# Kernel optimization log

Measured on AMD Instinct MI355X. Metric: run time of the kernel, lower is better.

Reference implementation:

```python
import jax, jax.numpy as jnp
import numpy as np

D_MODEL = 2048
N_HEADS = 16
D_K = D_MODEL // N_HEADS
MAX_SEQ = 2048
THETA = 10000.0


def _rope(x, token_positions):
    # x: [B, H, S, d_k], token_positions: [S] int
    freqs = 1.0 / THETA ** (jnp.arange(0, D_K, 2, dtype=jnp.float32) / D_K)  # [d_k/2]
    angles = token_positions.astype(jnp.float32)[:, None] * freqs[None, :]   # [S, d_k/2]
    cos, sin = jnp.cos(angles), jnp.sin(angles)
    x_even, x_odd = x[..., 0::2], x[..., 1::2]
    out_even = x_even * cos - x_odd * sin
    out_odd = x_even * sin + x_odd * cos
    return jnp.stack([out_even, out_odd], axis=-1).reshape(x.shape)


def setup_inputs() -> dict:
    key = jax.random.key(0)
    ks = jax.random.split(key, 5)
    B, S = 2, 2048
    std = np.sqrt(2.0 / (D_MODEL + D_MODEL))
    def w(k):
        return (jax.random.truncated_normal(k, -3.0, 3.0, (D_MODEL, D_MODEL), jnp.float32) * std)
    return {
        "x": jax.random.normal(ks[0], (B, S, D_MODEL), jnp.float32),
        "wq": w(ks[1]), "wk": w(ks[2]), "wv": w(ks[3]), "wo": w(ks[4]),
        "token_positions": jnp.arange(S, dtype=jnp.int32),
    }


def reference(x, wq, wk, wv, wo, token_positions):
    B, S, _ = x.shape
    # Linear: einsum('... i, o i -> ... o')
    def proj(w):
        h = jnp.einsum('bsi,oi->bso', x, w)
        return h.reshape(B, S, N_HEADS, D_K).transpose(0, 2, 1, 3)  # [B,H,S,d_k]
    Q, K, V = proj(wq), proj(wk), proj(wv)
    Q = _rope(Q, token_positions)
    K = _rope(K, token_positions)
    scores = jnp.einsum('bhqd,bhkd->bhqk', Q, K) / jnp.sqrt(jnp.float32(D_K))
    causal = jnp.tril(jnp.ones((S, S), dtype=bool))
    scores = jnp.where(causal, scores, -jnp.inf)
    attn = jax.nn.softmax(scores, axis=-1)
    out = jnp.einsum('bhqk,bhkd->bhqd', attn, V)
    out = out.transpose(0, 2, 1, 3).reshape(B, S, D_MODEL)
    return jnp.einsum('bsi,oi->bso', out, wo)
```

## Files before the change

### kernel.cpp

```cpp
#include <hip/hip_runtime.h>
#include <stdint.h>
#include <stddef.h>

typedef unsigned short u16;
typedef unsigned int u32;
typedef __attribute__((ext_vector_type(8))) short s8v;
typedef __attribute__((ext_vector_type(4))) short s4v;
typedef __attribute__((ext_vector_type(4))) float f4v;

#define D_MODEL 2048
#define NH 16
#define DK 128

__device__ __forceinline__ float b2f(u16 u) {
    union { u32 i; float f; } v; v.i = ((u32)u) << 16; return v.f;
}
__device__ __forceinline__ u16 f2b(float f) {
    u32 u = __builtin_bit_cast(u32, f);
    u32 r = (u + 0x7fffu + ((u >> 16) & 1u)) >> 16;
    return (u16)r;
}
__device__ __forceinline__ float fexp2(float x) {
    return __builtin_amdgcn_exp2f(x);
}
__device__ __forceinline__ f4v mfma16(s8v a, s8v b, f4v c) {
    return __builtin_amdgcn_mfma_f32_16x16x32_bf16(a, b, c, 0, 0, 0);
}
__device__ __forceinline__ void gload_lds16(const void* g, void* l) {
    __builtin_amdgcn_global_load_lds(
        (const __attribute__((address_space(1))) u32*)(uintptr_t)g,
        (__attribute__((address_space(3))) u32*)(uintptr_t)l, 16, 0, 0);
}

__device__ __forceinline__ void store_out(u16* p, float v)   { *p = f2b(v); }
__device__ __forceinline__ void store_out(float* p, float v) { *p = v; }

#define SBAR()   asm volatile("s_barrier" ::: "memory")
#define VMCNT(n) asm volatile("s_waitcnt vmcnt(" #n ")" ::: "memory")

__global__ __launch_bounds__(256) void cvt_bf16(
    const float* __restrict__ s0, const float* __restrict__ s1,
    const float* __restrict__ s2, const float* __restrict__ s3,
    const float* __restrict__ s4,
    u16* __restrict__ d0, u16* __restrict__ d1, u16* __restrict__ d2,
    u16* __restrict__ d3, u16* __restrict__ d4,
    int n0, int nw)
{
    const int seg = blockIdx.y;
    const float* s = (seg == 0) ? s0 : (seg == 1) ? s1 : (seg == 2) ? s2 : (seg == 3) ? s3 : s4;
    u16*         d = (seg == 0) ? d0 : (seg == 1) ? d1 : (seg == 2) ? d2 : (seg == 3) ? d3 : d4;
    const int    n = (seg == 0) ? n0 : nw;
    int i = (blockIdx.x * 256 + threadIdx.x) * 8;
    if (i >= n) return;
    f4v a = *(const f4v*)(s + i);
    f4v b = *(const f4v*)(s + i + 4);
    s8v o;
    o[0] = (short)f2b(a[0]); o[1] = (short)f2b(a[1]);
    o[2] = (short)f2b(a[2]); o[3] = (short)f2b(a[3]);
    o[4] = (short)f2b(b[0]); o[5] = (short)f2b(b[1]);
    o[6] = (short)f2b(b[2]); o[7] = (short)f2b(b[3]);
    *(s8v*)(d + i) = o;
}

__global__ __launch_bounds__(512) void gemm256(
    const u16* __restrict__ A,
    const u16* __restrict__ B0, const u16* __restrict__ B1,
    u16* __restrict__ C0, u16* __restrict__ C1,
    int M, int N, int K)
{
    const int z = blockIdx.z;
    const u16* Bp = (z == 0) ? B0 : B1;
    u16*       Cp = (z == 0) ? C0 : C1;

    __shared__ short As[2 * 256 * 64];
    __shared__ short Bs[2 * 256 * 64];

    const int t    = threadIdx.x;
    const int lane = t & 63;
    const int w    = t >> 6;
    const int wr   = w >> 2;
    const int wc   = w & 3;
    const int m0   = blockIdx.x * 256;
    const int n0   = blockIdx.y * 256;

    const int srow = t >> 3;
    const int scol = (((t & 7) ^ ((t >> 3) & 7)) * 8);

    const u16* gA = A  + (size_t)(m0 + srow) * K + scol;
    const u16* gB = Bp + (size_t)(n0 + srow) * K + scol;
    char* lA = (char*)As + (size_t)w * 1024;
    char* lB = (char*)Bs + (size_t)w * 1024;
    const size_t rstep = (size_t)64 * K;

    const int fr = lane & 15;
    const int g4 = lane >> 4;
    const int xa = fr & 7;

    f4v acc[8][4];
#pragma unroll
    for (int i = 0; i < 8; i++)
#pragma unroll
        for (int j = 0; j < 4; j++) acc[i][j] = (f4v){0.f, 0.f, 0.f, 0.f};

    auto stageA = [&](int p, int kt, int h) {
        const u16* g = gA + (size_t)kt * 64;
#pragma unroll
        for (int j = 0; j < 2; j++)
            gload_lds16(g + (size_t)(2 * h + j) * rstep,
                        lA + p * 32768 + (2 * h + j) * 8192);
    };
    auto stageB = [&](int p, int kt, int h) {
        const u16* g = gB + (size_t)kt * 64;
#pragma unroll
        for (int j = 0; j < 2; j++)
            gload_lds16(g + (size_t)(2 * h + j) * rstep,
                        lB + p * 32768 + (2 * h + j) * 8192);
    };
    auto loadA = [&](int p, int mh, int ks, s8v* aF) {
        const short* base = As + p * 16384;
        const int sl = ((ks * 4 + g4) ^ xa) * 8;
#pragma unroll
        for (int mi = 0; mi < 4; mi++)
            aF[mi] = *(const s8v*)&base[(wr * 128 + mh * 64 + mi * 16 + fr) * 64 + sl];
    };
    auto loadB = [&](int p, int ks, s8v* bF) {
        const short* base = Bs + p * 16384;
        const int sl = ((ks * 4 + g4) ^ xa) * 8;
#pragma unroll
        for (int ni = 0; ni < 4; ni++)
            bF[ni] = *(const s8v*)&base[(wc * 64 + ni * 16 + fr) * 64 + sl];
    };
    auto mfc = [&](int mh, s8v* aF, s8v* bF) {
        __builtin_amdgcn_s_setprio(1);
#pragma unroll
        for (int mi = 0; mi < 4; mi++)
#pragma unroll
            for (int ni = 0; ni < 4; ni++)
                acc[mh * 4 + mi][ni] = mfma16(aF[mi], bF[ni], acc[mh * 4 + mi][ni]);
        __builtin_amdgcn_s_setprio(0);
    };

    const int NT = K / 64;
    const int NI = NT / 2;

    stageB(0, 0, 0); stageB(0, 0, 1); stageA(0, 0, 0); stageA(0, 0, 1);
    stageB(1, 1, 0);
    VMCNT(2);
    SBAR();

    for (int i = 0; i < NI; i++) {
        const int k1 = 2 * i + 1;
        const int k2 = (2 * i + 2 < NT) ? 2 * i + 2 : 0;
        const int k3 = (2 * i + 3 < NT) ? 2 * i + 3 : 1;
        s8v aF[4], bF[4];

        loadA(0, 0, 0, aF); loadB(0, 0, bF);
        stageB(1, k1, 1);
        VMCNT(4); SBAR();
        mfc(0, aF, bF);
        SBAR();
        loadA(0, 1, 0, aF);
        stageA(1, k1, 0);
        SBAR();
        mfc(1, aF, bF);
        SBAR();
        loadA(0, 0, 1, aF); loadB(0, 1, bF);
        stageA(1, k1, 1);
        SBAR();
        mfc(0, aF, bF);
        SBAR();
        loadA(0, 1, 1, aF);
        stageB(0, k2, 0);
        VMCNT(2); SBAR();
        mfc(1, aF, bF);
        SBAR();
        loadA(1, 0, 0, aF); loadB(1, 0, bF);
        stageB(0, k2, 1);
        VMCNT(4); SBAR();
        mfc(0, aF, bF);
        SBAR();
        loadA(1, 1, 0, aF);
        stageA(0, k2, 0);
        SBAR();
        mfc(1, aF, bF);
        SBAR();
        loadA(1, 0, 1, aF); loadB(1, 1, bF);
        stageA(0, k2, 1);
        SBAR();
        mfc(0, aF, bF);
        SBAR();
        loadA(1, 1, 1, aF);
        stageB(1, k3, 0);
        VMCNT(2); SBAR();
        mfc(1, aF, bF);
        SBAR();
    }
    VMCNT(0);

    const int rg = g4 * 4;
#pragma unroll
    for (int mit = 0; mit < 8; mit++)
#pragma unroll
        for (int ni = 0; ni < 4; ni++) {
            size_t base = (size_t)(m0 + wr * 128 + mit * 16 + rg) * N
                        + (n0 + wc * 64 + ni * 16 + fr);
#pragma unroll
            for (int r = 0; r < 4; r++)
                Cp[base + (size_t)r * N] = f2b(acc[mit][ni][r]);
        }
}

template<typename OutT, int MODE>
__global__ __launch_bounds__(512) void gemm128(
    const u16* __restrict__ A, const u16* __restrict__ Bp,
    OutT* __restrict__ Cp, int M, int N, int K, int Sdim)
{
    __shared__ short As[3 * 256 * 64];
    __shared__ short Bs[3 * 128 * 64];

    const int t    = threadIdx.x;
    const int lane = t & 63;
    const int w    = t >> 6;
    const int wr   = w >> 1;
    const int wc   = w & 1;
    const int m0   = blockIdx.x * 256;
    const int n0   = blockIdx.y * 128;

    const int srow = t >> 3;
    const int scol = (((t & 7) ^ ((t >> 3) & 7)) * 8);

    const u16* gA = A  + (size_t)(m0 + srow) * K + scol;
    const u16* gB = Bp + (size_t)(n0 + srow) * K + scol;
    char* lA = (char*)As + (size_t)w * 1024;
    char* lB = (char*)Bs + (size_t)w * 1024;
    const size_t rstep = (size_t)64 * K;

    const int fr = lane & 15;
    const int g4 = lane >> 4;
    const int xa = fr & 7;

    f4v acc[4][4];
#pragma unroll
    for (int i = 0; i < 4; i++)
#pragma unroll
        for (int j = 0; j < 4; j++) acc[i][j] = (f4v){0.f, 0.f, 0.f, 0.f};

    auto stageA = [&](int p, int kt, int h) {
        const u16* g = gA + (size_t)kt * 64;
#pragma unroll
        for (int j = 0; j < 2; j++)
            gload_lds16(g + (size_t)(2 * h + j) * rstep,
                        lA + p * 32768 + (2 * h + j) * 8192);
    };
    auto stageB = [&](int p, int kt) {
        const u16* g = gB + (size_t)kt * 64;
#pragma unroll
        for (int j = 0; j < 2; j++)
            gload_lds16(g + (size_t)j * rstep,
                        lB + p * 16384 + j * 8192);
    };
    auto loadA = [&](int p, int mh, int ks, s8v* aF) {
        const short* base = As + p * 16384;
        const int sl = ((ks * 4 + g4) ^ xa) * 8;
#pragma unroll
        for (int j = 0; j < 2; j++)
            aF[j] = *(const s8v*)&base[(wr * 64 + (mh * 2 + j) * 16 + fr) * 64 + sl];
    };
    auto loadB = [&](int p, int ks, s8v* bF) {
        const short* base = Bs + p * 8192;
        const int sl = ((ks * 4 + g4) ^ xa) * 8;
#pragma unroll
        for (int ni = 0; ni < 4; ni++)
            bF[ni] = *(const s8v*)&base[(wc * 64 + ni * 16 + fr) * 64 + sl];
    };
    auto mfc = [&](int mh, s8v* aF, s8v* bF) {
        __builtin_amdgcn_s_setprio(1);
#pragma unroll
        for (int j = 0; j < 2; j++)
#pragma unroll
            for (int ni = 0; ni < 4; ni++)
                acc[mh * 2 + j][ni] = mfma16(aF[j], bF[ni], acc[mh * 2 + j][ni]);
        __builtin_amdgcn_s_setprio(0);
    };

    const int NT = K / 64;
    const int NI = NT / 2;

    stageA(0, 0, 0); stageA(0, 0, 1); stageB(0, 0);
    stageA(1, 1, 0); stageA(1, 1, 1); stageB(1, 1);
    VMCNT(6);
    SBAR();

    int s0 = 0, s1 = 1, s2 = 2;
    for (int i = 0; i < NI; i++) {
        const int k2 = (2 * i + 2 < NT) ? 2 * i + 2 : 0;
        const int k3 = (2 * i + 3 < NT) ? 2 * i + 3 : 1;
        s8v aF[2], bF[4];

        loadB(s0, 0, bF); loadA(s0, 0, 0, aF);
        stageA(s2, k2, 0);
        SBAR(); mfc(0, aF, bF); SBAR();
        loadA(s0, 1, 0, aF);
        stageA(s2, k2, 1);
        SBAR(); mfc(1, aF, bF); SBAR();
        loadB(s0, 1, bF); loadA(s0, 0, 1, aF);
        stageB(s2, k2);
        SBAR(); mfc(0, aF, bF); SBAR();
        loadA(s0, 1, 1, aF);
        VMCNT(6); SBAR(); mfc(1, aF, bF); SBAR();
        loadB(s1, 0, bF); loadA(s1, 0, 0, aF);
        stageA(s0, k3, 0);
        SBAR(); mfc(0, aF, bF); SBAR();
        loadA(s1, 1, 0, aF);
        stageA(s0, k3, 1);
        SBAR(); mfc(1, aF, bF); SBAR();
        loadB(s1, 1, bF); loadA(s1, 0, 1, aF);
        stageB(s0, k3);
        SBAR(); mfc(0, aF, bF); SBAR();
        loadA(s1, 1, 1, aF);
        VMCNT(6); SBAR(); mfc(1, aF, bF); SBAR();

        const int ns0 = s2, ns1 = s0, ns2 = s1;
        s0 = ns0; s1 = ns1; s2 = ns2;
    }
    VMCNT(0);

    const int rg = g4 * 4;
    if constexpr (MODE == 0) {
#pragma unroll
        for (int mi = 0; mi < 4; mi++)
#pragma unroll
            for (int ni = 0; ni < 4; ni++) {
                size_t base = (size_t)(m0 + wr * 64 + mi * 16 + rg) * N
                            + (n0 + wc * 64 + ni * 16 + fr);
#pragma unroll
                for (int r = 0; r < 4; r++)
                    store_out(&Cp[base + (size_t)r * N], acc[mi][ni][r]);
            }
    } else {
        __syncthreads();
        short* OT = As;
        const int OP = 264;
#pragma unroll
        for (int mi = 0; mi < 4; mi++)
#pragma unroll
            for (int ni = 0; ni < 4; ni++) {
                s4v pk;
                pk[0] = (short)f2b(acc[mi][ni][0]);
                pk[1] = (short)f2b(acc[mi][ni][1]);
                pk[2] = (short)f2b(acc[mi][ni][2]);
                pk[3] = (short)f2b(acc[mi][ni][3]);
                *(s4v*)&OT[(wc * 64 + ni * 16 + fr) * OP + (wr * 64 + mi * 16 + rg)] = pk;
            }
        __syncthreads();
        const int bb = m0 / Sdim;
        const int sb = m0 % Sdim;
        u16* Vt = (u16*)Cp;
#pragma unroll
        for (int ps = 0; ps < 8; ps++) {
            int idx  = ps * 512 + t;
            int orow = idx >> 5;
            int sc8  = (idx & 31) * 8;
            s8v v = *(const s8v*)&OT[orow * OP + sc8];
            *(s8v*)(Vt + ((size_t)bb * D_MODEL + n0 + orow) * Sdim + sb + sc8) = v;
        }
    }
}

__global__ void rope_kernel(u32* __restrict__ Q, u32* __restrict__ Kb,
                            const int* __restrict__ pos, int total, int S)
{
    int idx = blockIdx.x * 256 + threadIdx.x;
    if (idx >= total) return;
    int row = idx >> 10;
    int pr  = idx & 1023;
    int i   = pr & 63;
    int s   = row % S;
    float p    = (float)pos[s];
    float freq = __expf((float)i * -0.14391156831212787f);
    float ang  = p * freq;
    float c = cosf(ang), sn = sinf(ang);

    u32 qp = Q[idx];
    float qe = b2f((u16)(qp & 0xffffu)), qo = b2f((u16)(qp >> 16));
    const float sc = 0.12751919968793342f;
    float qe2 = (qe * c - qo * sn) * sc;
    float qo2 = (qe * sn + qo * c) * sc;
    Q[idx] = (u32)f2b(qe2) | ((u32)f2b(qo2) << 16);

    u32 kp = Kb[idx];
    float ke = b2f((u16)(kp & 0xffffu)), ko = b2f((u16)(kp >> 16));
    float ke2 = ke * c - ko * sn;
    float ko2 = ke * sn + ko * c;
    Kb[idx] = (u32)f2b(ke2) | ((u32)f2b(ko2) << 16);
}

#define AKV 64
#define VP  72
#define PP  72

__global__ __launch_bounds__(512) void attn_kernel(
    const u16* __restrict__ Qg, const u16* __restrict__ Kg,
    const u16* __restrict__ Vtg, u16* __restrict__ Og, int S)
{
    __shared__ short Kbuf[2][64 * 128];
    __shared__ short Vbuf[2][128 * VP];
    __shared__ short Ps[8][16 * PP];

    const int t    = threadIdx.x;
    const int lane = t & 63;
    const int w    = t >> 6;
    const int fr   = lane & 15;
    const int g4   = lane >> 4;
    const int xfr  = (fr & 7) << 3;

    const int d_ = blockIdx.x;
    const int tt = d_ >> 3;
    const int G  = ((tt & 3) << 3) | (d_ & 7);
    const int p  = tt >> 2;
    const int h  = G & 15;
    const int b  = G >> 4;
    const int ntq = S / 128;

    const u16* Qb  = Qg + ((size_t)b * S) * D_MODEL + (size_t)h * DK;
    const u16* Kb  = Kg + ((size_t)b * S) * D_MODEL + (size_t)h * DK;
    const u16* Vtb = Vtg + ((size_t)b * D_MODEL + (size_t)h * DK) * S;
    u16*       Ob  = Og + ((size_t)b * S) * D_MODEL + (size_t)h * DK;

    const int krow = t >> 4;
    const int kc8  = (t & 15) * 8;
    const int kxor = (krow & 7) << 3;
    const int vd   = t >> 3;
    const int vk8  = (t & 7) * 8;

    const int wq64 = (w >> 2) * 64;

    for (int half = 0; half < 2; half++) {
        const int T   = half ? (ntq - 1 - p) : p;
        const int q0  = T * 128;
        const int nkv = 2 * T + 2;

        s8v qf[4];
#pragma unroll
        for (int ks = 0; ks < 4; ks++)
            qf[ks] = *(const s8v*)(Qb +
                (size_t)(q0 + w * 16 + fr) * D_MODEL + ks * 32 + g4 * 8);

        s8v kreg[2], vreg[2];
#pragma unroll
        for (int c = 0; c < 2; c++) {
            kreg[c] = *(const s8v*)(Kb + (size_t)(krow + 32 * c) * D_MODEL + kc8);
            vreg[c] = *(const s8v*)(Vtb + (size_t)(vd + 64 * c) * S + vk8);
        }
        __syncthreads();
#pragma unroll
        for (int c = 0; c < 2; c++)
            *(s8v*)&Kbuf[0][(krow + 32 * c) * 128 + (kc8 ^ kxor)] = kreg[c];
#pragma unroll
        for (int c = 0; c < 2; c++)
            *(s8v*)&Vbuf[0][(vd + 64 * c) * VP + vk8] = vreg[c];
        __syncthreads();

        float m_st = -1e30f, l_st = 0.f;
        f4v accO[8];
#pragma unroll
        for (int df = 0; df < 8; df++) accO[df] = (f4v){0.f, 0.f, 0.f, 0.f};
        const int qg = q0 + w * 16 + fr;

        for (int kt = 0; kt < nkv; kt++) {
            const int  kv0  = kt * AKV;
            const int  buf  = kt & 1;
            const bool last = (kt + 1 == nkv);
            const bool act  = (kv0 <= q0 + wq64);

            if (!last) {
                const size_t kvn = (size_t)(kt + 1) * AKV;
#pragma unroll
                for (int c = 0; c < 2; c++) {
                    kreg[c] = *(const s8v*)(Kb + (kvn + krow + 32 * c) * D_MODEL + kc8);
                    vreg[c] = *(const s8v*)(Vtb + (size_t)(vd + 64 * c) * S + kvn + vk8);
                }
            }

            if (act) {
                f4v sacc[4];
#pragma unroll
                for (int i = 0; i < 4; i++) sacc[i] = (f4v){0.f, 0.f, 0.f, 0.f};
#pragma unroll
                for (int ks = 0; ks < 4; ks++) {
#pragma unroll
                    for (int kf = 0; kf < 4; kf++) {
                        s8v kfr = *(const s8v*)&Kbuf[buf][(kf * 16 + fr) * 128 +
                                                         ((ks * 32 + g4 * 8) ^ xfr)];
                        sacc[kf] = mfma16(kfr, qf[ks], sacc[kf]);
                    }
                }

                if (kv0 == q0 + wq64) {
#pragma unroll
                    for (int kf = 0; kf < 4; kf++)
#pragma unroll
                        for (int r = 0; r < 4; r++)
                            if (kv0 + kf * 16 + g4 * 4 + r > qg)
                                sacc[kf][r] = -1e30f;
                }
                float rm = -1e30f;
#pragma unroll
                for (int kf = 0; kf < 4; kf++)
                    rm = fmaxf(rm, fmaxf(fmaxf(sacc[kf][0], sacc[kf][1]),
                                         fmaxf(sacc[kf][2], sacc[kf][3])));
                rm = fmaxf(rm, __shfl_xor(rm, 16));
                rm = fmaxf(rm, __shfl_xor(rm, 32));
                if (__any(rm > m_st)) {
                    float mn   = fmaxf(m_st, rm);
                    float corr = fexp2(m_st - mn);
                    l_st *= corr;
#pragma unroll
                    for (int df = 0; df < 8; df++) {
                        accO[df][0] *= corr; accO[df][1] *= corr;
                        accO[df][2] *= corr; accO[df][3] *= corr;
                    }
                    m_st = mn;
                }
                float rsum = 0.f;
#pragma unroll
                for (int kf = 0; kf < 4; kf++) {
                    float p0 = fexp2(sacc[kf][0] - m_st);
                    float p1 = fexp2(sacc[kf][1] - m_st);
                    float p2 = fexp2(sacc[kf][2] - m_st);
                    float p3 = fexp2(sacc[kf][3] - m_st);
                    rsum += (p0 + p1) + (p2 + p3);
                    s4v pk;
                    pk[0] = (short)f2b(p0); pk[1] = (short)f2b(p1);
                    pk[2] = (short)f2b(p2); pk[3] = (short)f2b(p3);
                    *(s4v*)&Ps[w][fr * PP + kf * 16 + g4 * 4] = pk;
                }
                rsum += __shfl_xor(rsum, 16);
                rsum += __shfl_xor(rsum, 32);
                l_st += rsum;

#pragma unroll
                for (int ks = 0; ks < 2; ks++) {
                    s8v pf = *(const s8v*)&Ps[w][fr * PP + ks * 32 + g4 * 8];
#pragma unroll
                    for (int df = 0; df < 8; df++) {
                        s8v vf = *(const s8v*)&Vbuf[buf][(df * 16 + fr) * VP +
                                                         ks * 32 + g4 * 8];
                        accO[df] = mfma16(vf, pf, accO[df]);
                    }
                }
            }

            if (!last) {
#pragma unroll
                for (int c = 0; c < 2; c++)
                    *(s8v*)&Kbuf[buf ^ 1][(krow + 32 * c) * 128 + (kc8 ^ kxor)] = kreg[c];
#pragma unroll
                for (int c = 0; c < 2; c++)
                    *(s8v*)&Vbuf[buf ^ 1][(vd + 64 * c) * VP + vk8] = vreg[c];
            }
            __syncthreads();
        }

        float inv = 1.f / l_st;
        short* OL = (short*)&Kbuf[0][0];
#pragma unroll
        for (int df = 0; df < 8; df++) {
            s4v ov;
            ov[0] = (short)f2b(accO[df][0] * inv);
            ov[1] = (short)f2b(accO[df][1] * inv);
            ov[2] = (short)f2b(accO[df][2] * inv);
            ov[3] = (short)f2b(accO[df][3] * inv);
            *(s4v*)&OL[(w * 16 + fr) * 128 + ((df * 16 + g4 * 4) ^ xfr)] = ov;
        }
        __syncthreads();
#pragma unroll
        for (int i = 0; i < 4; i++) {
            int row = i * 32 + (t >> 4);
            int ch  = (t & 15) * 8;
            s8v v = *(const s8v*)&OL[row * 128 + (ch ^ ((row & 7) << 3))];
            *(s8v*)(Ob + (size_t)(q0 + row) * D_MODEL + ch) = v;
        }
    }
}

extern "C" void kernel_launch(void* const* d_in, const int* in_sizes, int n_in,
                              void* d_out, int out_size, void* d_ws, size_t ws_size,
                              hipStream_t stream)
{
    const float* x  = (const float*)d_in[0];
    const float* wq = (const float*)d_in[1];
    const float* wk = (const float*)d_in[2];
    const float* wv = (const float*)d_in[3];
    const float* wo = (const float*)d_in[4];
    const int*   tp = (const int*)d_in[5];

    const int S  = in_sizes[5];
    const int BS = in_sizes[0] / D_MODEL;
    const int Bn = BS / S;
    const int NW = D_MODEL * D_MODEL;
    const int NX = BS * D_MODEL;

    u16* Qw  = (u16*)d_ws;
    u16* Kw  = Qw + (size_t)NX;
    u16* Vw  = Kw + (size_t)NX;
    u16* Xb  = Vw + (size_t)NX;
    u16* Wqb = Xb + (size_t)NX;
    u16* Wkb = Wqb + (size_t)NW;
    u16* Wvb = Wkb + (size_t)NW;
    u16* Wob = Wvb + (size_t)NW;

    {
        dim3 g((NX / 8 + 255) / 256, 5);
        cvt_bf16<<<g, 256, 0, stream>>>(x, wq, wk, wv, wo,
                                        Xb, Wqb, Wkb, Wvb, Wob, NX, NW);
    }

    dim3 gqk(BS / 256, D_MODEL / 256, 2);
    gemm256<<<gqk, 512, 0, stream>>>(Xb, Wqb, Wkb, Qw, Kw, BS, D_MODEL, D_MODEL);

    dim3 gv(BS / 256, D_MODEL / 128, 1);
    gemm128<u16, 1><<<gv, 512, 0, stream>>>(Xb, Wvb, Vw, BS, D_MODEL, D_MODEL, S);

    int total = BS * (D_MODEL / 2);
    rope_kernel<<<(total + 255) / 256, 256, 0, stream>>>((u32*)Qw, (u32*)Kw, tp, total, S);

    attn_kernel<<<dim3((S / 256) * NH * Bn, 1, 1), 512, 0, stream>>>(Qw, Kw, Vw, Xb, S);

    dim3 go(BS / 256, D_MODEL / 128, 1);
    gemm128<float, 0><<<go, 512, 0, stream>>>(Xb, Wob, (float*)d_out,
                                              BS, D_MODEL, D_MODEL, S);
}
```

Measured before the change: 237.2 us.

## Assign 256-query tiles per attention block with two Q subtiles per warp

Each attention block now processes a single 256-row query tile instead of a balanced pair of 128-row tiles. Each warp handles 32 query rows as two 16-row subtiles, so every K and V fragment read from LDS feeds two MFMAs, which halves LDS traffic per unit of compute. Shared memory becomes one flat buffer with explicit offsets, and the output staging is reused for a 256-row write-out. The cost is that the earlier pairing of short and long causal tiles is lost, so blocks differ widely in work and the longest block grows. Each warp also holds twice as many accumulator registers.

```diff
diff --git a/kernel.cpp b/kernel.cpp
--- a/kernel.cpp
+++ b/kernel.cpp
@@ -403,9 +403,11 @@
     const u16* __restrict__ Qg, const u16* __restrict__ Kg,
     const u16* __restrict__ Vtg, u16* __restrict__ Og, int S)
 {
-    __shared__ short Kbuf[2][64 * 128];
-    __shared__ short Vbuf[2][128 * VP];
-    __shared__ short Ps[8][16 * PP];
+    __shared__ short smem[16384 + 18432 + 18432];
+    short* Kbf = smem;
+    short* Vbf = smem + 16384;
+    short* Psb = smem + 16384 + 18432;
+    short* OL  = smem;
 
     const int t    = threadIdx.x;
     const int lane = t & 63;
@@ -417,10 +419,9 @@
     const int d_ = blockIdx.x;
     const int tt = d_ >> 3;
     const int G  = ((tt & 3) << 3) | (d_ & 7);
-    const int p  = tt >> 2;
+    const int T  = tt >> 2;
     const int h  = G & 15;
     const int b  = G >> 4;
-    const int ntq = S / 128;
 
     const u16* Qb  = Qg + ((size_t)b * S) * D_MODEL + (size_t)h * DK;
     const u16* Kb  = Kg + ((size_t)b * S) * D_MODEL + (size_t)h * DK;
@@ -433,154 +434,174 @@
     const int vd   = t >> 3;
     const int vk8  = (t & 7) * 8;
 
-    const int wq64 = (w >> 2) * 64;
-
-    for (int half = 0; half < 2; half++) {
-        const int T   = half ? (ntq - 1 - p) : p;
-        const int q0  = T * 128;
-        const int nkv = 2 * T + 2;
-
-        s8v qf[4];
+    const int q0b = T * 256;
+    const int nkv = 4 * T + 4;
+    const int q0w = q0b + w * 32;
+    short* Pw = Psb + w * (32 * PP);
+
+    s8v qf[2][4];
+#pragma unroll
+    for (int s = 0; s < 2; s++)
 #pragma unroll
         for (int ks = 0; ks < 4; ks++)
-            qf[ks] = *(const s8v*)(Qb +
-                (size_t)(q0 + w * 16 + fr) * D_MODEL + ks * 32 + g4 * 8);
-
-        s8v kreg[2], vreg[2];
-#pragma unroll
-        for (int c = 0; c < 2; c++) {
-            kreg[c] = *(const s8v*)(Kb + (size_t)(krow + 32 * c) * D_MODEL + kc8);
-            vreg[c] = *(const s8v*)(Vtb + (size_t)(vd + 64 * c) * S + vk8);
+            qf[s][ks] = *(const s8v*)(Qb +
+                (size_t)(q0w + s * 16 + fr) * D_MODEL + ks * 32 + g4 * 8);
+
+    s8v kreg[2], vreg[2];
+#pragma unroll
+    for (int c = 0; c < 2; c++) {
+        kreg[c] = *(const s8v*)(Kb + (size_t)(krow + 32 * c) * D_MODEL + kc8);
+        vreg[c] = *(const s8v*)(Vtb + (size_t)(vd + 64 * c) * S + vk8);
+    }
+#pragma unroll
+    for (int c = 0; c < 2; c++)
+        *(s8v*)&Kbf[(krow + 32 * c) * 128 + (kc8 ^ kxor)] = kreg[c];
+#pragma unroll
+    for (int c = 0; c < 2; c++)
+        *(s8v*)&Vbf[(vd + 64 * c) * VP + vk8] = vreg[c];
+    __syncthreads();
+
+    float m_st[2] = {-1e30f, -1e30f};
+    float l_st[2] = {0.f, 0.f};
+    f4v accO[2][8];
+#pragma unroll
+    for (int s = 0; s < 2; s++)
+#pragma unroll
+        for (int df = 0; df < 8; df++) accO[s][df] = (f4v){0.f, 0.f, 0.f, 0.f};
+
+    for (int kt = 0; kt < nkv; kt++) {
+        const int  kv0  = kt * AKV;
+        const int  buf  = kt & 1;
+        const bool last = (kt + 1 == nkv);
+        const bool act  = (kv0 < q0w + 32);
+
+        if (!last) {
+            const size_t kvn = (size_t)(kt + 1) * AKV;
+#pragma unroll
+            for (int c = 0; c < 2; c++) {
+                kreg[c] = *(const s8v*)(Kb + (kvn + krow + 32 * c) * D_MODEL + kc8);
+                vreg[c] = *(const s8v*)(Vtb + (size_t)(vd + 64 * c) * S + kvn + vk8);
+            }
         }
-        __syncthreads();
-#pragma unroll
-        for (int c = 0; c < 2; c++)
-            *(s8v*)&Kbuf[0][(krow + 32 * c) * 128 + (kc8 ^ kxor)] = kreg[c];
-#pragma unroll
-        for (int c = 0; c < 2; c++)
-            *(s8v*)&Vbuf[0][(vd + 64 * c) * VP + vk8] = vreg[c];
-        __syncthreads();
-
-        float m_st = -1e30f, l_st = 0.f;
-        f4v accO[8];
-#pragma unroll
-        for (int df = 0; df < 8; df++) accO[df] = (f4v){0.f, 0.f, 0.f, 0.f};
-        const int qg = q0 + w * 16 + fr;
-
-        for (int kt = 0; kt < nkv; kt++) {
-            const int  kv0  = kt * AKV;
-            const int  buf  = kt & 1;
-            const bool last = (kt + 1 == nkv);
-            const bool act  = (kv0 <= q0 + wq64);
-
-            if (!last) {
-                const size_t kvn = (size_t)(kt + 1) * AKV;
-#pragma unroll
-                for (int c = 0; c < 2; c++) {
-                    kreg[c] = *(const s8v*)(Kb + (kvn + krow + 32 * c) * D_MODEL + kc8);
-                    vreg[c] = *(const s8v*)(Vtb + (size_t)(vd + 64 * c) * S + kvn + vk8);
-                }
+
+        if (act) {
+            const short* Kcur = Kbf + buf * 8192;
+            const short* Vcur = Vbf + buf * 9216;
+
+            f4v sacc[2][4];
+#pragma unroll
+            for (int s = 0; s < 2; s++)
+#pragma unroll
+                for (int i = 0; i < 4; i++) sacc[s][i] = (f4v){0.f, 0.f, 0.f, 0.f};
+#pragma unroll
+            for (int ks = 0; ks < 4; ks++) {
+                s8v kfr[4];
+#pragma unroll
+                for (int kf = 0; kf < 4; kf++)
+                    kfr[kf] = *(const s8v*)&Kcur[(kf * 16 + fr) * 128 +
+                                                 ((ks * 32 + g4 * 8) ^ xfr)];
+#pragma unroll
+                for (int kf = 0; kf < 4; kf++)
+                    sacc[0][kf] = mfma16(kfr[kf], qf[0][ks], sacc[0][kf]);
+#pragma unroll
+                for (int kf = 0; kf < 4; kf++)
+                    sacc[1][kf] = mfma16(kfr[kf], qf[1][ks], sacc[1][kf]);
             }
 
-            if (act) {
-                f4v sacc[4];
-#pragma unroll
-                for (int i = 0; i < 4; i++) sacc[i] = (f4v){0.f, 0.f, 0.f, 0.f};
-#pragma unroll
-                for (int ks = 0; ks < 4; ks++) {
-#pragma unroll
-                    for (int kf = 0; kf < 4; kf++) {
-                        s8v kfr = *(const s8v*)&Kbuf[buf][(kf * 16 + fr) * 128 +
-                                                         ((ks * 32 + g4 * 8) ^ xfr)];
-                        sacc[kf] = mfma16(kfr, qf[ks], sacc[kf]);
-                    }
-                }
-
-                if (kv0 == q0 + wq64) {
+            const bool dmask = (kv0 + AKV > q0w);
+#pragma unroll
+            for (int s = 0; s < 2; s++) {
+                const int qg = q0w + s * 16 + fr;
+                if (dmask) {
 #pragma unroll
                     for (int kf = 0; kf < 4; kf++)
 #pragma unroll
                         for (int r = 0; r < 4; r++)
                             if (kv0 + kf * 16 + g4 * 4 + r > qg)
-                                sacc[kf][r] = -1e30f;
+                                sacc[s][kf][r] = -1e30f;
                 }
                 float rm = -1e30f;
 #pragma unroll
                 for (int kf = 0; kf < 4; kf++)
-                    rm = fmaxf(rm, fmaxf(fmaxf(sacc[kf][0], sacc[kf][1]),
-                                         fmaxf(sacc[kf][2], sacc[kf][3])));
+                    rm = fmaxf(rm, fmaxf(fmaxf(sacc[s][kf][0], sacc[s][kf][1]),
+                                         fmaxf(sacc[s][kf][2], sacc[s][kf][3])));
                 rm = fmaxf(rm, __shfl_xor(rm, 16));
                 rm = fmaxf(rm, __shfl_xor(rm, 32));
-                if (__any(rm > m_st)) {
-                    float mn   = fmaxf(m_st, rm);
-                    float corr = fexp2(m_st - mn);
-                    l_st *= corr;
+                if (__any(rm > m_st[s])) {
+                    float mn   = fmaxf(m_st[s], rm);
+                    float corr = fexp2(m_st[s] - mn);
+                    l_st[s] *= corr;
 #pragma unroll
                     for (int df = 0; df < 8; df++) {
-                        accO[df][0] *= corr; accO[df][1] *= corr;
-                        accO[df][2] *= corr; accO[df][3] *= corr;
+                        accO[s][df][0] *= corr; accO[s][df][1] *= corr;
+                        accO[s][df][2] *= corr; accO[s][df][3] *= corr;
                     }
-                    m_st = mn;
+                    m_st[s] = mn;
                 }
                 float rsum = 0.f;
 #pragma unroll
                 for (int kf = 0; kf < 4; kf++) {
-                    float p0 = fexp2(sacc[kf][0] - m_st);
-                    float p1 = fexp2(sacc[kf][1] - m_st);
-                    float p2 = fexp2(sacc[kf][2] - m_st);
-                    float p3 = fexp2(sacc[kf][3] - m_st);
+                    float p0 = fexp2(sacc[s][kf][0] - m_st[s]);
+                    float p1 = fexp2(sacc[s][kf][1] - m_st[s]);
+                    float p2 = fexp2(sacc[s][kf][2] - m_st[s]);
+                    float p3 = fexp2(sacc[s][kf][3] - m_st[s]);
                     rsum += (p0 + p1) + (p2 + p3);
                     s4v pk;
                     pk[0] = (short)f2b(p0); pk[1] = (short)f2b(p1);
                     pk[2] = (short)f2b(p2); pk[3] = (short)f2b(p3);
-                    *(s4v*)&Ps[w][fr * PP + kf * 16 + g4 * 4] = pk;
+                    *(s4v*)&Pw[(s * 16 + fr) * PP + kf * 16 + g4 * 4] = pk;
                 }
                 rsum += __shfl_xor(rsum, 16);
                 rsum += __shfl_xor(rsum, 32);
-                l_st += rsum;
-
-#pragma unroll
-                for (int ks = 0; ks < 2; ks++) {
-                    s8v pf = *(const s8v*)&Ps[w][fr * PP + ks * 32 + g4 * 8];
-#pragma unroll
-                    for (int df = 0; df < 8; df++) {
-                        s8v vf = *(const s8v*)&Vbuf[buf][(df * 16 + fr) * VP +
-                                                         ks * 32 + g4 * 8];
-                        accO[df] = mfma16(vf, pf, accO[df]);
-                    }
+                l_st[s] += rsum;
+            }
+
+#pragma unroll
+            for (int ks = 0; ks < 2; ks++) {
+                s8v pf0 = *(const s8v*)&Pw[fr * PP + ks * 32 + g4 * 8];
+                s8v pf1 = *(const s8v*)&Pw[(16 + fr) * PP + ks * 32 + g4 * 8];
+#pragma unroll
+                for (int df = 0; df < 8; df++) {
+                    s8v vf = *(const s8v*)&Vcur[(df * 16 + fr) * VP +
+                                                ks * 32 + g4 * 8];
+                    accO[0][df] = mfma16(vf, pf0, accO[0][df]);
+                    accO[1][df] = mfma16(vf, pf1, accO[1][df]);
                 }
             }
-
-            if (!last) {
-#pragma unroll
-                for (int c = 0; c < 2; c++)
-                    *(s8v*)&Kbuf[buf ^ 1][(krow + 32 * c) * 128 + (kc8 ^ kxor)] = kreg[c];
-#pragma unroll
-                for (int c = 0; c < 2; c++)
-                    *(s8v*)&Vbuf[buf ^ 1][(vd + 64 * c) * VP + vk8] = vreg[c];
-            }
-            __syncthreads();
         }
 
-        float inv = 1.f / l_st;
-        short* OL = (short*)&Kbuf[0][0];
+        if (!last) {
+#pragma unroll
+            for (int c = 0; c < 2; c++)
+                *(s8v*)&Kbf[(buf ^ 1) * 8192 + (krow + 32 * c) * 128 + (kc8 ^ kxor)] = kreg[c];
+#pragma unroll
+            for (int c = 0; c < 2; c++)
+                *(s8v*)&Vbf[(buf ^ 1) * 9216 + (vd + 64 * c) * VP + vk8] = vreg[c];
+        }
+        __syncthreads();
+    }
+
+#pragma unroll
+    for (int s = 0; s < 2; s++) {
+        float inv = 1.f / l_st[s];
 #pragma unroll
         for (int df = 0; df < 8; df++) {
             s4v ov;
-            ov[0] = (short)f2b(accO[df][0] * inv);
-            ov[1] = (short)f2b(accO[df][1] * inv);
-            ov[2] = (short)f2b(accO[df][2] * inv);
-            ov[3] = (short)f2b(accO[df][3] * inv);
-            *(s4v*)&OL[(w * 16 + fr) * 128 + ((df * 16 + g4 * 4) ^ xfr)] = ov;
+            ov[0] = (short)f2b(accO[s][df][0] * inv);
+            ov[1] = (short)f2b(accO[s][df][1] * inv);
+            ov[2] = (short)f2b(accO[s][df][2] * inv);
+            ov[3] = (short)f2b(accO[s][df][3] * inv);
+            *(s4v*)&OL[(w * 32 + s * 16 + fr) * 128 + ((df * 16 + g4 * 4) ^ xfr)] = ov;
         }
-        __syncthreads();
-#pragma unroll
-        for (int i = 0; i < 4; i++) {
-            int row = i * 32 + (t >> 4);
-            int ch  = (t & 15) * 8;
-            s8v v = *(const s8v*)&OL[row * 128 + (ch ^ ((row & 7) << 3))];
-            *(s8v*)(Ob + (size_t)(q0 + row) * D_MODEL + ch) = v;
-        }
+    }
+    __syncthreads();
+#pragma unroll
+    for (int ps = 0; ps < 8; ps++) {
+        int idx = ps * 512 + t;
+        int row = idx >> 4;
+        int ch  = (idx & 15) * 8;
+        s8v v = *(const s8v*)&OL[row * 128 + (ch ^ ((row & 7) << 3))];
+        *(s8v*)(Ob + (size_t)(q0b + row) * D_MODEL + ch) = v;
     }
 }
 
```

New measurement: 261.3 us. 10.2% more time.

## Fuse RoPE into QK projection epilogue via precomputed cos/sin table; prioritize attention MFMA

Applied to the files above, without the earlier changes.

Removes the standalone RoPE kernel. A small kernel now precomputes a cos/sin table per position and frequency, and the Q/K GEMM epilogue applies the rotation and the Q scaling before the bf16 store. It gets each pair partner through a lane shuffle, since adjacent columns sit in adjacent lanes. This saves a full read-modify-write pass over Q and K. Separately, s_setprio raises wave priority around the MFMA loops in attention. The cost is extra epilogue work and table loads inside the GEMM.

```diff
diff --git a/kernel.cpp b/kernel.cpp
--- a/kernel.cpp
+++ b/kernel.cpp
@@ -62,10 +62,23 @@
     *(s8v*)(d + i) = o;
 }
 
+__global__ __launch_bounds__(256) void rope_table(
+    float2* __restrict__ tab, const int* __restrict__ pos, int S)
+{
+    int idx = blockIdx.x * 256 + threadIdx.x;
+    if (idx >= S * 64) return;
+    int s  = idx >> 6;
+    int ip = idx & 63;
+    float freq = __expf((float)ip * -0.14391156831212787f);
+    float ang  = (float)pos[s] * freq;
+    tab[idx] = make_float2(cosf(ang), sinf(ang));
+}
+
 __global__ __launch_bounds__(512) void gemm256(
     const u16* __restrict__ A,
     const u16* __restrict__ B0, const u16* __restrict__ B1,
     u16* __restrict__ C0, u16* __restrict__ C1,
+    const float2* __restrict__ rtab, int Sdim,
     int M, int N, int K)
 {
     const int z = blockIdx.z;
@@ -198,15 +211,26 @@
     VMCNT(0);
 
     const int rg = g4 * 4;
+    const float scale = (z == 0) ? 0.12751919968793342f : 1.0f;
+    const int srow_b = (m0 % Sdim) + wr * 128;
 #pragma unroll
     for (int mit = 0; mit < 8; mit++)
 #pragma unroll
         for (int ni = 0; ni < 4; ni++) {
-            size_t base = (size_t)(m0 + wr * 128 + mit * 16 + rg) * N
-                        + (n0 + wc * 64 + ni * 16 + fr);
-#pragma unroll
-            for (int r = 0; r < 4; r++)
-                Cp[base + (size_t)r * N] = f2b(acc[mit][ni][r]);
+            const int col = n0 + wc * 64 + ni * 16 + fr;
+            const int ip  = (col & 127) >> 1;
+            const int odd = col & 1;
+            size_t base = (size_t)(m0 + wr * 128 + mit * 16 + rg) * N + col;
+            const int sr = srow_b + mit * 16 + rg;
+#pragma unroll
+            for (int r = 0; r < 4; r++) {
+                float2 cs = rtab[(size_t)(sr + r) * 64 + ip];
+                float v  = acc[mit][ni][r];
+                float pv = __shfl_xor(v, 1);
+                float o  = odd ? (pv * cs.y + v * cs.x)
+                               : (v * cs.x - pv * cs.y);
+                Cp[base + (size_t)r * N] = f2b(o * scale);
+            }
         }
 }
 
@@ -367,34 +391,6 @@
     }
 }
 
-__global__ void rope_kernel(u32* __restrict__ Q, u32* __restrict__ Kb,
-                            const int* __restrict__ pos, int total, int S)
-{
-    int idx = blockIdx.x * 256 + threadIdx.x;
-    if (idx >= total) return;
-    int row = idx >> 10;
-    int pr  = idx & 1023;
-    int i   = pr & 63;
-    int s   = row % S;
-    float p    = (float)pos[s];
-    float freq = __expf((float)i * -0.14391156831212787f);
-    float ang  = p * freq;
-    float c = cosf(ang), sn = sinf(ang);
-
-    u32 qp = Q[idx];
-    float qe = b2f((u16)(qp & 0xffffu)), qo = b2f((u16)(qp >> 16));
-    const float sc = 0.12751919968793342f;
-    float qe2 = (qe * c - qo * sn) * sc;
-    float qo2 = (qe * sn + qo * c) * sc;
-    Q[idx] = (u32)f2b(qe2) | ((u32)f2b(qo2) << 16);
-
-    u32 kp = Kb[idx];
-    float ke = b2f((u16)(kp & 0xffffu)), ko = b2f((u16)(kp >> 16));
-    float ke2 = ke * c - ko * sn;
-    float ko2 = ke * sn + ko * c;
-    Kb[idx] = (u32)f2b(ke2) | ((u32)f2b(ko2) << 16);
-}
-
 #define AKV 64
 #define VP  72
 #define PP  72
@@ -486,6 +482,7 @@
                 f4v sacc[4];
 #pragma unroll
                 for (int i = 0; i < 4; i++) sacc[i] = (f4v){0.f, 0.f, 0.f, 0.f};
+                __builtin_amdgcn_s_setprio(1);
 #pragma unroll
                 for (int ks = 0; ks < 4; ks++) {
 #pragma unroll
@@ -495,6 +492,7 @@
                         sacc[kf] = mfma16(kfr, qf[ks], sacc[kf]);
                     }
                 }
+                __builtin_amdgcn_s_setprio(0);
 
                 if (kv0 == q0 + wq64) {
 #pragma unroll
@@ -539,6 +537,7 @@
                 rsum += __shfl_xor(rsum, 32);
                 l_st += rsum;
 
+                __builtin_amdgcn_s_setprio(1);
 #pragma unroll
                 for (int ks = 0; ks < 2; ks++) {
                     s8v pf = *(const s8v*)&Ps[w][fr * PP + ks * 32 + g4 * 8];
@@ -549,6 +548,7 @@
                         accO[df] = mfma16(vf, pf, accO[df]);
                     }
                 }
+                __builtin_amdgcn_s_setprio(0);
             }
 
             if (!last) {
@@ -609,6 +609,7 @@
     u16* Wkb = Wqb + (size_t)NW;
     u16* Wvb = Wkb + (size_t)NW;
     u16* Wob = Wvb + (size_t)NW;
+    float2* Rt = (float2*)(Wob + (size_t)NW);
 
     {
         dim3 g((NX / 8 + 255) / 256, 5);
@@ -616,14 +617,14 @@
                                         Xb, Wqb, Wkb, Wvb, Wob, NX, NW);
     }
 
+    rope_table<<<(S * 64 + 255) / 256, 256, 0, stream>>>(Rt, tp, S);
+
     dim3 gqk(BS / 256, D_MODEL / 256, 2);
-    gemm256<<<gqk, 512, 0, stream>>>(Xb, Wqb, Wkb, Qw, Kw, BS, D_MODEL, D_MODEL);
+    gemm256<<<gqk, 512, 0, stream>>>(Xb, Wqb, Wkb, Qw, Kw, Rt, S,
+                                     BS, D_MODEL, D_MODEL);
 
     dim3 gv(BS / 256, D_MODEL / 128, 1);
     gemm128<u16, 1><<<gv, 512, 0, stream>>>(Xb, Wvb, Vw, BS, D_MODEL, D_MODEL, S);
-
-    int total = BS * (D_MODEL / 2);
-    rope_kernel<<<(total + 255) / 256, 256, 0, stream>>>((u32*)Qw, (u32*)Kw, tp, total, S);
 
     attn_kernel<<<dim3((S / 256) * NH * Bn, 1, 1), 512, 0, stream>>>(Qw, Kw, Vw, Xb, S);
 
```

New measurement: 229.8 us (median of 2 runs). 1.03x faster.
